# Optimization experiments

Hardware: AMD Instinct MI355X
Metric: run time of the kernel (lower is better)

The kernel has to match this reference:

```python
import jax, jax.numpy as jnp
import numpy as np
from jax import lax

NEG_SLOPE = 0.01  # torch LeakyReLU default
PAD = 2           # (5-1)//2


def _depthwise_conv1d(x, w, b):
    # x: [B, C, L], w: [C, 1, K] (one filter per channel), b: [C]
    C = x.shape[1]
    y = lax.conv_general_dilated(
        x, w,
        window_strides=(1,),
        padding=[(PAD, PAD)],
        dimension_numbers=("NCH", "OIH", "NCH"),
        feature_group_count=C,
    )
    return y + b[None, :, None]


def setup_inputs() -> dict:
    key = jax.random.key(0)
    k1, k2, k3, k4, k5 = jax.random.split(key, 5)
    B, C, L, K = 128, 20, 10000, 5
    # fan_in for Conv1d(1,1,5) is 5 -> torch init bound = 1/sqrt(5)
    bound = 1.0 / np.sqrt(K)
    x = jax.random.normal(k1, (B, C, L), dtype=jnp.float32)
    w1 = jax.random.uniform(k2, (C, 1, K), jnp.float32, -bound, bound)
    b1 = jax.random.uniform(k3, (C,), jnp.float32, -bound, bound)
    w2 = jax.random.uniform(k4, (C, 1, K), jnp.float32, -bound, bound)
    b2 = jax.random.uniform(k5, (C,), jnp.float32, -bound, bound)
    return {"x": x, "w1": w1, "b1": b1, "w2": w2, "b2": b2}


def reference(x, w1, b1, w2, b2):
    # Equivalent to the per-channel Python loop: each channel c runs
    # conv1d(1->1) -> LeakyReLU -> conv1d(1->1) -> sigmoid, then gates x.
    h = _depthwise_conv1d(x, w1, b1)
    h = jnp.where(h >= 0, h, NEG_SLOPE * h)
    att = jax.nn.sigmoid(_depthwise_conv1d(h, w2, b2))
    return x * att
```

## Files before the change

### kernel.cpp

```cpp
#include <hip/hip_runtime.h>
#include <math.h>

#define BLOCK 256
#define VEC   4
#define TILE  (BLOCK * VEC)
#define KW    5

__global__ __launch_bounds__(BLOCK) void wav_attn_kernel(
    const float* __restrict__ x,
    const float* __restrict__ w1,
    const float* __restrict__ b1,
    const float* __restrict__ w2,
    const float* __restrict__ b2,
    float* __restrict__ out,
    int C, int L)
{
    const int row = blockIdx.y;
    const int c   = row % C;
    const long long base = (long long)row * L;
    const int i   = blockIdx.x * TILE + threadIdx.x * VEC;
    if (i >= L) return;

    float W1[KW], W2[KW];
    #pragma unroll
    for (int k = 0; k < KW; ++k) {
        W1[k] = w1[c * KW + k];
        W2[k] = w2[c * KW + k];
    }
    const float B1 = b1[c];
    const float B2 = b2[c];

    float a[12];
    if (i >= 4 && i + 7 < L) {
        float4 v0 = *reinterpret_cast<const float4*>(x + base + i - 4);
        float4 v1 = *reinterpret_cast<const float4*>(x + base + i);
        float4 v2 = *reinterpret_cast<const float4*>(x + base + i + 4);
        a[0] = v0.x; a[1] = v0.y; a[2]  = v0.z; a[3]  = v0.w;
        a[4] = v1.x; a[5] = v1.y; a[6]  = v1.z; a[7]  = v1.w;
        a[8] = v2.x; a[9] = v2.y; a[10] = v2.z; a[11] = v2.w;
    } else {
        #pragma unroll
        for (int e = 0; e < 12; ++e) {
            int g = i - 4 + e;
            a[e] = (g >= 0 && g < L) ? x[base + g] : 0.f;
        }
    }

    float h[8];
    #pragma unroll
    for (int j = 0; j < 8; ++j) {
        int p = i + j - 2;
        float acc = B1;
        #pragma unroll
        for (int k = 0; k < KW; ++k)
            acc = fmaf(W1[k], a[j + k], acc);
        acc = (acc >= 0.f) ? acc : 0.01f * acc;
        h[j] = (p >= 0 && p < L) ? acc : 0.f;
    }

    float res[4];
    #pragma unroll
    for (int e = 0; e < 4; ++e) {
        float z = B2;
        #pragma unroll
        for (int k = 0; k < KW; ++k)
            z = fmaf(W2[k], h[e + k], z);
        float s = __builtin_amdgcn_rcpf(1.f + __expf(-z));
        res[e] = a[4 + e] * s;
    }

    if (i + 3 < L) {
        *reinterpret_cast<float4*>(out + base + i) =
            make_float4(res[0], res[1], res[2], res[3]);
    } else {
        #pragma unroll
        for (int e = 0; e < 4; ++e)
            if (i + e < L) out[base + i + e] = res[e];
    }
}

extern "C" void kernel_launch(void* const* d_in, const int* in_sizes, int n_in,
                              void* d_out, int out_size, void* d_ws, size_t ws_size,
                              hipStream_t stream) {
    const float* x  = (const float*)d_in[0];
    const float* w1 = (const float*)d_in[1];
    const float* b1 = (const float*)d_in[2];
    const float* w2 = (const float*)d_in[3];
    const float* b2 = (const float*)d_in[4];
    float* out = (float*)d_out;

    const int C = in_sizes[2];
    const int B = 128;
    const int L = in_sizes[0] / (B * C);

    dim3 grid((L + TILE - 1) / TILE, B * C);
    wav_attn_kernel<<<grid, BLOCK, 0, stream>>>(x, w1, b1, w2, b2, out, C, L);
}
```

Measured before the change: 180.9 us.

## Process multiple tiles per block with register double-buffered prefetch

Each block now handles five consecutive tiles of a row, loading the next tile's inputs into registers while computing and storing the current one. This is meant to hide global-load latency and amortize per-block weight/bias loads and launch overhead. It reduces the grid size fivefold and raises register use, which may lower occupancy or leave fewer blocks to balance across CUs.

After: 191.3 us. +5.7%, slower.

```diff
diff --git a/kernel.cpp b/kernel.cpp
--- a/kernel.cpp
+++ b/kernel.cpp
@@ -5,6 +5,63 @@
 #define VEC   4
 #define TILE  (BLOCK * VEC)
 #define KW    5
+#define TPB   5
+
+typedef float f32x4 __attribute__((ext_vector_type(4)));
+
+__device__ __forceinline__ void load_tile(const float* __restrict__ xr,
+                                          int i, int L, float a[12]) {
+    if (i >= 4 && i + 7 < L) {
+        f32x4 v0 = *reinterpret_cast<const f32x4*>(xr + i - 4);
+        f32x4 v1 = *reinterpret_cast<const f32x4*>(xr + i);
+        f32x4 v2 = *reinterpret_cast<const f32x4*>(xr + i + 4);
+        #pragma unroll
+        for (int e = 0; e < 4; ++e) {
+            a[e] = v0[e]; a[4 + e] = v1[e]; a[8 + e] = v2[e];
+        }
+    } else {
+        #pragma unroll
+        for (int e = 0; e < 12; ++e) {
+            int g = i - 4 + e;
+            a[e] = (g >= 0 && g < L) ? xr[g] : 0.f;
+        }
+    }
+}
+
+__device__ __forceinline__ void compute_store(const float a[12], int i, int L,
+                                              const float* W1, float B1,
+                                              const float* W2, float B2,
+                                              float* __restrict__ outr) {
+    float h[8];
+    #pragma unroll
+    for (int j = 0; j < 8; ++j) {
+        int p = i + j - 2;
+        float acc = B1;
+        #pragma unroll
+        for (int k = 0; k < KW; ++k)
+            acc = fmaf(W1[k], a[j + k], acc);
+        acc = (acc >= 0.f) ? acc : 0.01f * acc;
+        h[j] = (p >= 0 && p < L) ? acc : 0.f;
+    }
+    float res[4];
+    #pragma unroll
+    for (int e = 0; e < 4; ++e) {
+        float z = B2;
+        #pragma unroll
+        for (int k = 0; k < KW; ++k)
+            z = fmaf(W2[k], h[e + k], z);
+        float s = __builtin_amdgcn_rcpf(1.f + __expf(-z));
+        res[e] = a[4 + e] * s;
+    }
+    if (i + 3 < L) {
+        f32x4 r = { res[0], res[1], res[2], res[3] };
+        *reinterpret_cast<f32x4*>(outr + i) = r;
+    } else {
+        #pragma unroll
+        for (int e = 0; e < 4; ++e)
+            if (i + e < L) outr[i + e] = res[e];
+    }
+}
 
 __global__ __launch_bounds__(BLOCK) void wav_attn_kernel(
     const float* __restrict__ x,
@@ -17,9 +74,8 @@
 {
     const int row = blockIdx.y;
     const int c   = row % C;
-    const long long base = (long long)row * L;
-    const int i   = blockIdx.x * TILE + threadIdx.x * VEC;
-    if (i >= L) return;
+    const float* xr   = x   + (long long)row * L;
+    float*       outr = out + (long long)row * L;
 
     float W1[KW], W2[KW];
     #pragma unroll
@@ -30,52 +86,21 @@
     const float B1 = b1[c];
     const float B2 = b2[c];
 
-    float a[12];
-    if (i >= 4 && i + 7 < L) {
-        float4 v0 = *reinterpret_cast<const float4*>(x + base + i - 4);
-        float4 v1 = *reinterpret_cast<const float4*>(x + base + i);
-        float4 v2 = *reinterpret_cast<const float4*>(x + base + i + 4);
-        a[0] = v0.x; a[1] = v0.y; a[2]  = v0.z; a[3]  = v0.w;
-        a[4] = v1.x; a[5] = v1.y; a[6]  = v1.z; a[7]  = v1.w;
-        a[8] = v2.x; a[9] = v2.y; a[10] = v2.z; a[11] = v2.w;
-    } else {
+    int i = (blockIdx.x * TPB) * TILE + threadIdx.x * VEC;
+
+    float aCur[12], aNxt[12] = {};
+    load_tile(xr, i, L, aCur);
+
+    #pragma unroll
+    for (int t = 0; t < TPB; ++t) {
+        const int iN = i + TILE;
+        if (t + 1 < TPB)
+            load_tile(xr, iN, L, aNxt);
+        if (i < L)
+            compute_store(aCur, i, L, W1, B1, W2, B2, outr);
         #pragma unroll
-        for (int e = 0; e < 12; ++e) {
-            int g = i - 4 + e;
-            a[e] = (g >= 0 && g < L) ? x[base + g] : 0.f;
-        }
-    }
-
-    float h[8];
-    #pragma unroll
-    for (int j = 0; j < 8; ++j) {
-        int p = i + j - 2;
-        float acc = B1;
-        #pragma unroll
-        for (int k = 0; k < KW; ++k)
-            acc = fmaf(W1[k], a[j + k], acc);
-        acc = (acc >= 0.f) ? acc : 0.01f * acc;
-        h[j] = (p >= 0 && p < L) ? acc : 0.f;
-    }
-
-    float res[4];
-    #pragma unroll
-    for (int e = 0; e < 4; ++e) {
-        float z = B2;
-        #pragma unroll
-        for (int k = 0; k < KW; ++k)
-            z = fmaf(W2[k], h[e + k], z);
-        float s = __builtin_amdgcn_rcpf(1.f + __expf(-z));
-        res[e] = a[4 + e] * s;
-    }
-
-    if (i + 3 < L) {
-        *reinterpret_cast<float4*>(out + base + i) =
-            make_float4(res[0], res[1], res[2], res[3]);
-    } else {
-        #pragma unroll
-        for (int e = 0; e < 4; ++e)
-            if (i + e < L) out[base + i + e] = res[e];
+        for (int e = 0; e < 12; ++e) aCur[e] = aNxt[e];
+        i = iN;
     }
 }
 
@@ -93,6 +118,7 @@
     const int B = 128;
     const int L = in_sizes[0] / (B * C);
 
-    dim3 grid((L + TILE - 1) / TILE, B * C);
+    const int nTiles = (L + TILE - 1) / TILE;
+    dim3 grid((nTiles + TPB - 1) / TPB, B * C);
     wav_attn_kernel<<<grid, BLOCK, 0, stream>>>(x, w1, b1, w2, b2, out, C, L);
 }
```
